# Kernel optimization log

Hardware: AMD Instinct MI355X
Metric: run time of the kernel (lower is better)

## Reference

```python
import jax, jax.numpy as jnp
import numpy as np

B, G, D, N_HEADS, FFN, L = 16, 2048, 256, 8, 1024, 4
HEAD_DIM = D // N_HEADS
EPS_LN = 1e-5
MASK_TOKEN = -10.0
REE_BASE = 100.0


def setup_inputs() -> dict:
    key = jax.random.key(0)
    ks = jax.random.split(key, 20)
    s = 0.02
    inp = {
        'x': jax.random.normal(ks[0], (B, G), jnp.float32),
        'gene_emb': jax.random.normal(ks[1], (G, D), jnp.float32) * s,
        'inv_freq': (1.0 / REE_BASE ** (jnp.arange(0, D, 2, dtype=jnp.float32) / D)),
        'Wq': jax.random.normal(ks[2], (L, D, D), jnp.float32) * s,
        'bq': jnp.zeros((L, D), jnp.float32),
        'Wk': jax.random.normal(ks[3], (L, D, D), jnp.float32) * s,
        'bk': jnp.zeros((L, D), jnp.float32),
        'Wv': jax.random.normal(ks[4], (L, D, D), jnp.float32) * s,
        'bv': jnp.zeros((L, D), jnp.float32),
        'ln1_g': jnp.ones((L, D), jnp.float32),
        'ln1_b': jnp.zeros((L, D), jnp.float32),
        'ln2_g': jnp.ones((L, D), jnp.float32),
        'ln2_b': jnp.zeros((L, D), jnp.float32),
        'WU': jax.random.normal(ks[5], (L, D, FFN), jnp.float32) * s,
        'bU': jnp.zeros((L, FFN), jnp.float32),
        'WV': jax.random.normal(ks[6], (L, FFN, D), jnp.float32) * s,
        'bV': jnp.zeros((L, D), jnp.float32),
        'Wout': jax.random.normal(ks[7], (D, 1), jnp.float32) * s,
        'bout': jnp.zeros((1,), jnp.float32),
    }
    return inp


def layernorm(x, g, b):
    m = x.mean(-1, keepdims=True)
    v = ((x - m) ** 2).mean(-1, keepdims=True)
    return (x - m) / jnp.sqrt(v + EPS_LN) * g + b


def causal_linear_attention(q, k, v):
    # q, k already feature-mapped ('sqr'); shapes [B, S, H, dh]
    b, s, h, dh = q.shape
    qs, ks_, vs = (jnp.moveaxis(t, 1, 0) for t in (q, k, v))  # [S,B,H,dh]
    num0 = jnp.zeros((b, h, dh, dh), q.dtype)
    den0 = jnp.zeros((b, h, dh), q.dtype)

    def step(carry, qkv):
        num_s, den_s = carry
        qt, kt, vt = qkv
        num_s = num_s + jnp.einsum('bhf,bhd->bhfd', kt, vt)
        den_s = den_s + kt
        num = jnp.einsum('bhf,bhfd->bhd', qt, num_s)
        den = jnp.einsum('bhf,bhf->bh', qt, den_s)
        return (num_s, den_s), num / (den[..., None] + 1e-16)

    _, out = jax.lax.scan(step, (num0, den0), (qs, ks_, vs))  # [S,B,H,dh]
    return jnp.moveaxis(out, 0, 1).reshape(b, s, h * dh)


def reference(x, gene_emb, inv_freq, Wq, bq, Wk, bk, Wv, bv,
              ln1_g, ln1_b, ln2_g, ln2_b, WU, bU, WV, bV, Wout, bout):
    b, g = x.shape
    # Rotary Expression Embedding
    freqs = x[..., None] * inv_freq  # [B,G,D/2]
    emb = jnp.concatenate([jnp.sin(freqs), jnp.cos(freqs)], axis=-1)  # [B,G,D]
    emb = jnp.where((x == MASK_TOKEN)[..., None], 0.0, emb)
    h = gene_emb[None] + emb  # [B,G,D]

    for l in range(Wq.shape[0]):
        hn = layernorm(h, ln1_g[l], ln1_b[l])  # pre-LN (on_gptln=True)
        q = (hn @ Wq[l] + bq[l]).reshape(b, g, N_HEADS, HEAD_DIM) ** 2
        k = (hn @ Wk[l] + bk[l]).reshape(b, g, N_HEADS, HEAD_DIM) ** 2
        v = (hn @ Wv[l] + bv[l]).reshape(b, g, N_HEADS, HEAD_DIM)
        h = h + causal_linear_attention(q, k, v)
        hn2 = layernorm(h, ln2_g[l], ln2_b[l])
        h = h + jax.nn.gelu(hn2 @ WU[l] + bU[l], approximate=False) @ WV[l] + bV[l]
    return (h @ Wout + bout).squeeze(-1)  # [B,G]
```

## Files before the change

### kernel.cpp

```cpp
#include <hip/hip_runtime.h>
#include <math.h>


#define GG 2048
#define DD 256
#define NROWS 32768
#define NC 32
#define CS 64

typedef __attribute__((ext_vector_type(8))) short bf16x8;
typedef __attribute__((ext_vector_type(4))) float f32x4;

__device__ __forceinline__ short f2bf(float f) {
  union { float f; unsigned u; } v; v.f = f;
  unsigned r = v.u + 0x7FFFu + ((v.u >> 16) & 1u);
  return (short)(r >> 16);
}
__device__ __forceinline__ float bf2f(short s) {
  union { unsigned u; float f; } v; v.u = ((unsigned)(unsigned short)s) << 16;
  return v.f;
}
__device__ __forceinline__ void gld16(const short* g, short* l) {
  __builtin_amdgcn_global_load_lds(
      (const __attribute__((address_space(1))) void*)g,
      (__attribute__((address_space(3))) void*)l, 16, 0, 0);
}
__device__ __forceinline__ float fast_gelu(float x) {
  float y = 1.595769122f * (x + 0.044715f * x * x * x);
  return x / (1.0f + __expf(-y));
}

__global__ __launch_bounds__(256) void embed_kernel(
    const float* __restrict__ x, const float* __restrict__ ge,
    const float* __restrict__ invf, float* __restrict__ h) {
  int bg = blockIdx.x * 4 + (threadIdx.x >> 6);
  int g = bg & (GG - 1);
  int lane = threadIdx.x & 63;
  float xv = x[bg];
  int d = lane * 4;
  float4 e;
  if (lane < 32) {
    float4 f = *(const float4*)&invf[d];
    e.x = sinf(xv * f.x); e.y = sinf(xv * f.y);
    e.z = sinf(xv * f.z); e.w = sinf(xv * f.w);
  } else {
    float4 f = *(const float4*)&invf[d - 128];
    e.x = cosf(xv * f.x); e.y = cosf(xv * f.y);
    e.z = cosf(xv * f.z); e.w = cosf(xv * f.w);
  }
  if (xv == -10.0f) { e.x = 0.f; e.y = 0.f; e.z = 0.f; e.w = 0.f; }
  float4 gv = *(const float4*)&ge[(size_t)g * DD + d];
  float4 o; o.x = gv.x + e.x; o.y = gv.y + e.y; o.z = gv.z + e.z; o.w = gv.w + e.w;
  *(float4*)&h[(size_t)bg * DD + d] = o;
}

__global__ __launch_bounds__(256) void ln_tiled(
    const float* __restrict__ h, const float* __restrict__ gamma,
    const float* __restrict__ beta, short* __restrict__ outT) {
  __shared__ float mean_s[32], rstd_s[32];
  __shared__ float gls[256], bls[256];
  int r0 = blockIdx.x * 32;
  int tid = threadIdx.x;
  gls[tid] = gamma[tid]; bls[tid] = beta[tid];
  {
    int row = tid >> 3, seg = tid & 7;
    const float4* hp = (const float4*)(h + (size_t)(r0 + row) * DD + seg * 32);
    float s = 0.f, s2 = 0.f;
#pragma unroll
    for (int i = 0; i < 8; ++i) {
      float4 v = hp[i];
      s += v.x + v.y + v.z + v.w;
      s2 += v.x * v.x + v.y * v.y + v.z * v.z + v.w * v.w;
    }
    s += __shfl_xor(s, 1); s += __shfl_xor(s, 2); s += __shfl_xor(s, 4);
    s2 += __shfl_xor(s2, 1); s2 += __shfl_xor(s2, 2); s2 += __shfl_xor(s2, 4);
    if (seg == 0) {
      float mn = s * (1.0f / 256.0f);
      mean_s[row] = mn;
      rstd_s[row] = rsqrtf(s2 * (1.0f / 256.0f) - mn * mn + 1e-5f);
    }
  }
  __syncthreads();
  int row = tid & 31, kc8 = (tid >> 5) & 3, half = tid >> 7;
  float mn = mean_s[row], rs = rstd_s[row];
  size_t hrow = (size_t)(r0 + row) * DD;
  int trow = (r0 & 127) + row;
  short* tb = outT + (size_t)(r0 >> 7) * 8 * 4096 + (kc8 * 128 + trow) * 8;
#pragma unroll
  for (int j = 0; j < 4; ++j) {
    int kb = half * 4 + j;
    int k0 = kb * 32 + kc8 * 8;
    float4 x0 = *(const float4*)&h[hrow + k0];
    float4 x1 = *(const float4*)&h[hrow + k0 + 4];
    float4 g0 = *(const float4*)&gls[k0], g1 = *(const float4*)&gls[k0 + 4];
    float4 b0 = *(const float4*)&bls[k0], b1 = *(const float4*)&bls[k0 + 4];
    bf16x8 aw;
    aw[0] = f2bf((x0.x - mn) * rs * g0.x + b0.x);
    aw[1] = f2bf((x0.y - mn) * rs * g0.y + b0.y);
    aw[2] = f2bf((x0.z - mn) * rs * g0.z + b0.z);
    aw[3] = f2bf((x0.w - mn) * rs * g0.w + b0.w);
    aw[4] = f2bf((x1.x - mn) * rs * g1.x + b1.x);
    aw[5] = f2bf((x1.y - mn) * rs * g1.y + b1.y);
    aw[6] = f2bf((x1.z - mn) * rs * g1.z + b1.z);
    aw[7] = f2bf((x1.w - mn) * rs * g1.w + b1.w);
    *(bf16x8*)&tb[(size_t)kb * 4096] = aw;
  }
}

__global__ __launch_bounds__(256) void prep_weights(
    const float* __restrict__ Wq, const float* __restrict__ Wk,
    const float* __restrict__ Wv, const float* __restrict__ WU,
    const float* __restrict__ WV,
    short* __restrict__ TQ, short* __restrict__ TK, short* __restrict__ TV,
    short* __restrict__ TU, short* __restrict__ TVd) {
  int zz = blockIdx.z, l = blockIdx.y;
  const float* src; short* dst; int Kd, Nd;
  if (zz == 0) { src = Wq; dst = TQ; Kd = 256; Nd = 256; }
  else if (zz == 1) { src = Wk; dst = TK; Kd = 256; Nd = 256; }
  else if (zz == 2) { src = Wv; dst = TV; Kd = 256; Nd = 256; }
  else if (zz == 3) { src = WU; dst = TU; Kd = 256; Nd = 1024; }
  else { src = WV; dst = TVd; Kd = 1024; Nd = 256; }
  int tot = Kd * Nd;
  int e = blockIdx.x * 256 + threadIdx.x;
  if (e >= tot) return;
  int t = e >> 12;
  int cslot = (e >> 3) & 511;
  int elem = e & 7;
  int kc8 = cslot >> 7, rn = cslot & 127;
  int nKb = Kd >> 5;
  int nt = t / nKb, kb = t - nt * nKb;
  int n = nt * 128 + rn, k = kb * 32 + kc8 * 8 + elem;
  dst[(size_t)l * tot + e] = f2bf(src[(size_t)l * tot + (size_t)k * Nd + n]);
}

template <int K, int EPI>
__global__ __launch_bounds__(256) void gemm_t(
    const short* __restrict__ A, const short* __restrict__ B0,
    const short* __restrict__ B1, const short* __restrict__ B2,
    const float* __restrict__ bias0, const float* __restrict__ bias1,
    const float* __restrict__ bias2,
    short* __restrict__ o0, short* __restrict__ o1, short* __restrict__ o2,
    float* __restrict__ outf, int N) {
  __shared__ __align__(16) short As[2][4096];
  __shared__ __align__(16) short Bs[2][4096];
  constexpr int nIter = K / 32;
  int z = blockIdx.z;
  const short* Bt = (z == 0) ? B0 : (z == 1) ? B1 : B2;
  const float* bias = (z == 0) ? bias0 : (z == 1) ? bias1 : bias2;
  short* outz = (z == 0) ? o0 : (z == 1) ? o1 : o2;
  int m0 = blockIdx.x * 128, n0 = blockIdx.y * 128;
  int tid = threadIdx.x;
  int lane = tid & 63, w = tid >> 6;
  int q = lane >> 4, r = lane & 15;
  int wm = (w >> 1) * 64, wn = (w & 1) * 64;
  const short* At = A + (size_t)blockIdx.x * nIter * 4096;
  const short* Btl = Bt + (size_t)blockIdx.y * nIter * 4096;
  f32x4 vzero = {0.f, 0.f, 0.f, 0.f};
  f32x4 acc[4][4];
#pragma unroll
  for (int i = 0; i < 4; ++i)
#pragma unroll
    for (int j = 0; j < 4; ++j) acc[i][j] = vzero;

  int c0 = tid * 8, c1 = (tid + 256) * 8;
#pragma unroll
  for (int g = 0; g < 2; ++g) {
    gld16(At + g * 4096 + c0, &As[g][c0]);
    gld16(At + g * 4096 + c1, &As[g][c1]);
    gld16(Btl + g * 4096 + c0, &Bs[g][c0]);
    gld16(Btl + g * 4096 + c1, &Bs[g][c1]);
  }

  int abase = (q * 128 + wm + r) * 8;
  int bbase = (q * 128 + wn + r) * 8;

#pragma unroll
  for (int gi = 0; gi < nIter - 1; ++gi) {
    __builtin_amdgcn_s_waitcnt(0x0f74);
    __builtin_amdgcn_s_barrier();
    const int cur = gi & 1;
    bf16x8 af[4], bfr[4];
#pragma unroll
    for (int mt = 0; mt < 4; ++mt)
      af[mt] = *(const bf16x8*)&As[cur][abase + mt * 16 * 8];
#pragma unroll
    for (int nt = 0; nt < 4; ++nt)
      bfr[nt] = *(const bf16x8*)&Bs[cur][bbase + nt * 16 * 8];
#pragma unroll
    for (int mt = 0; mt < 4; ++mt)
#pragma unroll
      for (int nt = 0; nt < 4; ++nt)
        acc[mt][nt] = __builtin_amdgcn_mfma_f32_16x16x32_bf16(bfr[nt], af[mt], acc[mt][nt], 0, 0, 0);
    __builtin_amdgcn_s_waitcnt(0xc07f);
    __builtin_amdgcn_s_barrier();
    if (gi + 2 < nIter) {
      size_t kn = (size_t)(gi + 2) * 4096;
      gld16(At + kn + c0, &As[cur][c0]);
      gld16(At + kn + c1, &As[cur][c1]);
      gld16(Btl + kn + c0, &Bs[cur][c0]);
      gld16(Btl + kn + c1, &Bs[cur][c1]);
    }
  }
  {
    __builtin_amdgcn_s_waitcnt(0x0f70);
    __builtin_amdgcn_s_barrier();
    const int cur = (nIter - 1) & 1;
    bf16x8 af[4], bfr[4];
#pragma unroll
    for (int mt = 0; mt < 4; ++mt)
      af[mt] = *(const bf16x8*)&As[cur][abase + mt * 16 * 8];
#pragma unroll
    for (int nt = 0; nt < 4; ++nt)
      bfr[nt] = *(const bf16x8*)&Bs[cur][bbase + nt * 16 * 8];
#pragma unroll
    for (int mt = 0; mt < 4; ++mt)
#pragma unroll
      for (int nt = 0; nt < 4; ++nt)
        acc[mt][nt] = __builtin_amdgcn_mfma_f32_16x16x32_bf16(bfr[nt], af[mt], acc[mt][nt], 0, 0, 0);
  }

  float4 bias4[4];
#pragma unroll
  for (int nt = 0; nt < 4; ++nt) bias4[nt] = *(const float4*)&bias[n0 + wn + nt * 16 + q * 4];
#pragma unroll
  for (int mt = 0; mt < 4; ++mt) {
    int ml = wm + mt * 16 + r;
    int m = m0 + ml;
    size_t rowoff = (size_t)m * N + n0 + wn + q * 4;
#pragma unroll
    for (int nt = 0; nt < 4; ++nt) {
      f32x4 v = acc[mt][nt];
      v[0] += bias4[nt].x; v[1] += bias4[nt].y; v[2] += bias4[nt].z; v[3] += bias4[nt].w;
      if (EPI == 0) {
        if (z < 2) { v[0] *= v[0]; v[1] *= v[1]; v[2] *= v[2]; v[3] *= v[3]; }
        short4 o; o.x = f2bf(v[0]); o.y = f2bf(v[1]); o.z = f2bf(v[2]); o.w = f2bf(v[3]);
        *(short4*)&outz[rowoff + nt * 16] = o;
      } else if (EPI == 1) {
#pragma unroll
        for (int e = 0; e < 4; ++e) v[e] = fast_gelu(v[e]);
        short4 o; o.x = f2bf(v[0]); o.y = f2bf(v[1]); o.z = f2bf(v[2]); o.w = f2bf(v[3]);
        int n = n0 + wn + nt * 16 + q * 4;
        size_t ti = ((size_t)blockIdx.x * (N >> 5) + (n >> 5)) * 4096 +
                    (size_t)(((n >> 3) & 3) << 10) + (ml << 3) + (n & 7);
        *(short4*)&outz[ti] = o;
      } else {
        float4 cur4 = *(float4*)&outf[rowoff + nt * 16];
        cur4.x += v[0]; cur4.y += v[1]; cur4.z += v[2]; cur4.w += v[3];
        *(float4*)&outf[rowoff + nt * 16] = cur4;
      }
    }
  }
}

__global__ __launch_bounds__(256) void attn_chunk_kv(
    const short* __restrict__ Kb, const short* __restrict__ Vb,
    float* __restrict__ St, float* __restrict__ Zc) {
  __shared__ short Kt[4][32 * 72];
  __shared__ short Vt[4][32 * 72];
  int wid = threadIdx.x >> 6;
  int blk = blockIdx.x * 4 + wid;
  int c = blk & (NC - 1), bh = blk >> 5;
  int b = bh >> 3, hh = bh & 7;
  int lane = threadIdx.x & 63, q = lane >> 4, r = lane & 15;
  size_t rowbase = ((size_t)(b * GG + c * CS + lane)) * DD + hh * 32;
#pragma unroll
  for (int j = 0; j < 4; ++j) {
    bf16x8 kv = *(const bf16x8*)&Kb[rowbase + j * 8];
    bf16x8 vv = *(const bf16x8*)&Vb[rowbase + j * 8];
#pragma unroll
    for (int e = 0; e < 8; ++e) {
      Kt[wid][(j * 8 + e) * 72 + lane] = kv[e];
      Vt[wid][(j * 8 + e) * 72 + lane] = vv[e];
    }
  }
  __syncthreads();
  f32x4 vzero = {0.f, 0.f, 0.f, 0.f};
  f32x4 acc[2][2];
#pragma unroll
  for (int i = 0; i < 2; ++i)
#pragma unroll
    for (int j = 0; j < 2; ++j) acc[i][j] = vzero;
#pragma unroll
  for (int ks = 0; ks < 2; ++ks) {
    bf16x8 afr[2], bfr[2];
#pragma unroll
    for (int mt = 0; mt < 2; ++mt) afr[mt] = *(const bf16x8*)&Kt[wid][(mt * 16 + r) * 72 + ks * 32 + q * 8];
#pragma unroll
    for (int nt = 0; nt < 2; ++nt) bfr[nt] = *(const bf16x8*)&Vt[wid][(nt * 16 + r) * 72 + ks * 32 + q * 8];
#pragma unroll
    for (int mt = 0; mt < 2; ++mt)
#pragma unroll
      for (int nt = 0; nt < 2; ++nt)
        acc[mt][nt] = __builtin_amdgcn_mfma_f32_16x16x32_bf16(afr[mt], bfr[nt], acc[mt][nt], 0, 0, 0);
  }
  float* stp = St + ((size_t)bh * NC + c) * 1024;
#pragma unroll
  for (int mt = 0; mt < 2; ++mt)
#pragma unroll
    for (int nt = 0; nt < 2; ++nt)
      *(f32x4*)&stp[(nt * 16 + r) * 32 + mt * 16 + q * 4] = acc[mt][nt];
  if (lane < 32) {
    float s = 0.f;
#pragma unroll
    for (int j = 0; j < 8; ++j) {
      bf16x8 kr = *(const bf16x8*)&Kt[wid][lane * 72 + j * 8];
#pragma unroll
      for (int e = 0; e < 8; ++e) s += bf2f(kr[e]);
    }
    Zc[((size_t)bh * NC + c) * 32 + lane] = s;
  }
}

__global__ __launch_bounds__(1024) void attn_prefix(float* __restrict__ St, float* __restrict__ Zc) {
  int bh = blockIdx.x, i = threadIdx.x;
  float run = 0.f;
  float* p = St + (size_t)bh * NC * 1024 + i;
#pragma unroll
  for (int c = 0; c < NC; ++c) { float t = p[(size_t)c * 1024]; p[(size_t)c * 1024] = run; run += t; }
  if (i < 32) {
    float rz = 0.f;
    float* pz = Zc + (size_t)bh * NC * 32 + i;
#pragma unroll
    for (int c = 0; c < NC; ++c) { float t = pz[c * 32]; pz[c * 32] = rz; rz += t; }
  }
}

__global__ __launch_bounds__(256) void attn_intra(
    const short* __restrict__ Qb, const short* __restrict__ Kb,
    const short* __restrict__ Vb, const float* __restrict__ St,
    const float* __restrict__ Zc, float* __restrict__ h) {
  __shared__ short P[4][64 * 72];
  __shared__ short Vt[4][32 * 72];
  __shared__ float den[4][64];
  int wid = threadIdx.x >> 6;
  int blk = blockIdx.x * 4 + wid;
  int c = blk & (NC - 1), bh = blk >> 5;
  int b = bh >> 3, hh = bh & 7;
  int lane = threadIdx.x & 63, q = lane >> 4, r = lane & 15;
  size_t row0 = (size_t)b * GG + c * CS;

  const float* zp = Zc + ((size_t)bh * NC + c) * 32;
  float qz = 0.f;
  {
    size_t qoff = (row0 + lane) * DD + hh * 32;
#pragma unroll
    for (int j = 0; j < 4; ++j) {
      bf16x8 qv = *(const bf16x8*)&Qb[qoff + j * 8];
#pragma unroll
      for (int e = 0; e < 8; ++e) qz += bf2f(qv[e]) * zp[j * 8 + e];
    }
  }
  den[wid][lane] = qz;

  {
    size_t voff = (row0 + lane) * DD + hh * 32;
#pragma unroll
    for (int j = 0; j < 4; ++j) {
      bf16x8 vv = *(const bf16x8*)&Vb[voff + j * 8];
#pragma unroll
      for (int e = 0; e < 8; ++e) Vt[wid][(j * 8 + e) * 72 + lane] = vv[e];
    }
  }

  bf16x8 ak[4], bqf[4];
#pragma unroll
  for (int t4 = 0; t4 < 4; ++t4) {
    ak[t4]  = *(const bf16x8*)&Kb[(row0 + t4 * 16 + r) * DD + hh * 32 + q * 8];
    bqf[t4] = *(const bf16x8*)&Qb[(row0 + t4 * 16 + r) * DD + hh * 32 + q * 8];
  }
  f32x4 vzero = {0.f, 0.f, 0.f, 0.f};
  f32x4 pacc[4][4];
#pragma unroll
  for (int mt = 0; mt < 4; ++mt)
#pragma unroll
    for (int nt = 0; nt < 4; ++nt)
      pacc[mt][nt] = __builtin_amdgcn_mfma_f32_16x16x32_bf16(ak[mt], bqf[nt], vzero, 0, 0, 0);

  float rs[4] = {0.f, 0.f, 0.f, 0.f};
#pragma unroll
  for (int nt = 0; nt < 4; ++nt) {
    int t = nt * 16 + r;
#pragma unroll
    for (int mt = 0; mt < 4; ++mt) {
      short4 pk;
#pragma unroll
      for (int rr = 0; rr < 4; ++rr) {
        int s = mt * 16 + q * 4 + rr;
        float pv = (s <= t) ? pacc[mt][nt][rr] : 0.f;
        rs[nt] += pv;
        ((short*)&pk)[rr] = f2bf(pv);
      }
      *(short4*)&P[wid][t * 72 + mt * 16 + q * 4] = pk;
    }
  }
#pragma unroll
  for (int nt = 0; nt < 4; ++nt) {
    rs[nt] += __shfl_xor(rs[nt], 16);
    rs[nt] += __shfl_xor(rs[nt], 32);
  }
  __syncthreads();
  if (lane < 16) {
#pragma unroll
    for (int nt = 0; nt < 4; ++nt) den[wid][nt * 16 + lane] += rs[nt];
  }
  __syncthreads();

  f32x4 oacc[4][2];
#pragma unroll
  for (int mt = 0; mt < 4; ++mt)
#pragma unroll
    for (int nt2 = 0; nt2 < 2; ++nt2) oacc[mt][nt2] = vzero;
  const float* stp = St + ((size_t)bh * NC + c) * 1024;
#pragma unroll
  for (int nt2 = 0; nt2 < 2; ++nt2) {
    float4 s0 = *(const float4*)&stp[(nt2 * 16 + r) * 32 + q * 8];
    float4 s1 = *(const float4*)&stp[(nt2 * 16 + r) * 32 + q * 8 + 4];
    bf16x8 bs;
    bs[0] = f2bf(s0.x); bs[1] = f2bf(s0.y); bs[2] = f2bf(s0.z); bs[3] = f2bf(s0.w);
    bs[4] = f2bf(s1.x); bs[5] = f2bf(s1.y); bs[6] = f2bf(s1.z); bs[7] = f2bf(s1.w);
#pragma unroll
    for (int mt = 0; mt < 4; ++mt)
      oacc[mt][nt2] = __builtin_amdgcn_mfma_f32_16x16x32_bf16(bqf[mt], bs, oacc[mt][nt2], 0, 0, 0);
  }
#pragma unroll
  for (int ks = 0; ks < 2; ++ks) {
    bf16x8 ap[4];
#pragma unroll
    for (int mt = 0; mt < 4; ++mt)
      ap[mt] = *(const bf16x8*)&P[wid][(mt * 16 + r) * 72 + ks * 32 + q * 8];
#pragma unroll
    for (int nt2 = 0; nt2 < 2; ++nt2) {
      bf16x8 bv_ = *(const bf16x8*)&Vt[wid][(nt2 * 16 + r) * 72 + ks * 32 + q * 8];
#pragma unroll
      for (int mt = 0; mt < 4; ++mt)
        oacc[mt][nt2] = __builtin_amdgcn_mfma_f32_16x16x32_bf16(ap[mt], bv_, oacc[mt][nt2], 0, 0, 0);
    }
  }

#pragma unroll
  for (int mt = 0; mt < 4; ++mt) {
#pragma unroll
    for (int rr = 0; rr < 4; ++rr) {
      int t = mt * 16 + q * 4 + rr;
      float inv = 1.0f / (den[wid][t] + 1e-16f);
#pragma unroll
      for (int nt2 = 0; nt2 < 2; ++nt2) {
        int d = nt2 * 16 + r;
        size_t off = (row0 + t) * DD + hh * 32 + d;
        h[off] += oacc[mt][nt2][rr] * inv;
      }
    }
  }
}

__global__ __launch_bounds__(256) void out_proj(
    const float* __restrict__ h, const float* __restrict__ Wout,
    const float* __restrict__ bout, float* __restrict__ out) {
  int row = blockIdx.x * 4 + (threadIdx.x >> 6);
  int lane = threadIdx.x & 63;
  float4 a = *(const float4*)&h[(size_t)row * DD + lane * 4];
  float4 w = *(const float4*)&Wout[lane * 4];
  float s = a.x * w.x + a.y * w.y + a.z * w.z + a.w * w.w;
#pragma unroll
  for (int o = 1; o < 64; o <<= 1) s += __shfl_xor(s, o);
  if (lane == 0) out[row] = s + bout[0];
}

extern "C" void kernel_launch(void* const* d_in, const int* in_sizes, int n_in,
                              void* d_out, int out_size, void* d_ws, size_t ws_size,
                              hipStream_t stream) {
  const float* x    = (const float*)d_in[0];
  const float* ge   = (const float*)d_in[1];
  const float* invf = (const float*)d_in[2];
  const float* Wq   = (const float*)d_in[3];
  const float* bq   = (const float*)d_in[4];
  const float* Wk   = (const float*)d_in[5];
  const float* bk   = (const float*)d_in[6];
  const float* Wv   = (const float*)d_in[7];
  const float* bv   = (const float*)d_in[8];
  const float* ln1g = (const float*)d_in[9];
  const float* ln1b = (const float*)d_in[10];
  const float* ln2g = (const float*)d_in[11];
  const float* ln2b = (const float*)d_in[12];
  const float* WU   = (const float*)d_in[13];
  const float* bU   = (const float*)d_in[14];
  const float* WV   = (const float*)d_in[15];
  const float* bV   = (const float*)d_in[16];
  const float* Wout = (const float*)d_in[17];
  const float* bout = (const float*)d_in[18];
  float* out = (float*)d_out;

  char* ws = (char*)d_ws;
  float* h   = (float*)(ws + 0);
  short* hn  = (short*)(ws + 33554432);
  char*  R   = ws + 50331648;
  short* qb  = (short*)(R + 0);
  short* kb  = (short*)(R + 16777216);
  short* vb  = (short*)(R + 33554432);
  float* St  = (float*)(R + 50331648);
  float* Zc  = (float*)(R + 67108864);
  short* mid = (short*)(R + 0);
  char*  WT  = R + 67633152;
  short* TQ  = (short*)(WT + 0);
  short* TK  = (short*)(WT + 524288);
  short* TVq = (short*)(WT + 1048576);
  short* TU  = (short*)(WT + 1572864);
  short* TVd = (short*)(WT + 3670016);

  prep_weights<<<dim3(1024, 4, 5), 256, 0, stream>>>(Wq, Wk, Wv, WU, WV, TQ, TK, TVq, TU, TVd);
  embed_kernel<<<NROWS / 4, 256, 0, stream>>>(x, ge, invf, h);

  for (int l = 0; l < 4; ++l) {
    ln_tiled<<<NROWS / 32, 256, 0, stream>>>(h, ln1g + l * 256, ln1b + l * 256, hn);
    gemm_t<256, 0><<<dim3(256, 2, 3), 256, 0, stream>>>(
        hn, TQ + l * 65536, TK + l * 65536, TVq + l * 65536,
        bq + l * 256, bk + l * 256, bv + l * 256,
        qb, kb, vb, nullptr, 256);
    attn_chunk_kv<<<1024, 256, 0, stream>>>(kb, vb, St, Zc);
    attn_prefix<<<128, 1024, 0, stream>>>(St, Zc);
    attn_intra<<<1024, 256, 0, stream>>>(qb, kb, vb, St, Zc, h);
    ln_tiled<<<NROWS / 32, 256, 0, stream>>>(h, ln2g + l * 256, ln2b + l * 256, hn);
    gemm_t<256, 1><<<dim3(256, 8, 1), 256, 0, stream>>>(
        hn, TU + l * 262144, nullptr, nullptr,
        bU + l * 1024, nullptr, nullptr,
        mid, nullptr, nullptr, nullptr, 1024);
    gemm_t<1024, 2><<<dim3(256, 2, 1), 256, 0, stream>>>(
        mid, TVd + l * 262144, nullptr, nullptr,
        bV + l * 256, nullptr, nullptr,
        nullptr, nullptr, nullptr, h, 256);
  }
  out_proj<<<NROWS / 4, 256, 0, stream>>>(h, Wout, bout, out);
}
```

Baseline: 790.3 us.

## Triple-buffer GEMM K-loop, stage epilogues through LDS, head-major QKV layout

The GEMM main loop moves from double to triple buffering of A/B tiles in a single shared array, with the wait count chosen by how many tiles are still outstanding. The QKV epilogue now stages results in LDS and writes head-major [head][row][32] bf16 so the attention kernels read contiguous 64-byte rows. The residual-add epilogue also stages through LDS in two halves so the fp32 read-modify-write of h is done with full-row coalesced float4 accesses. The aim is to hide more load latency and coalesce global traffic, at the cost of more LDS (lower occupancy) and extra barriers in the epilogues.

Result: faster. 762.5 us (-3.5%).

```diff
diff --git a/kernel.cpp b/kernel.cpp
--- a/kernel.cpp
+++ b/kernel.cpp
@@ -141,8 +141,7 @@
     const float* __restrict__ bias2,
     short* __restrict__ o0, short* __restrict__ o1, short* __restrict__ o2,
     float* __restrict__ outf, int N) {
-  __shared__ __align__(16) short As[2][4096];
-  __shared__ __align__(16) short Bs[2][4096];
+  __shared__ __align__(16) short L[24576];
   constexpr int nIter = K / 32;
   int z = blockIdx.z;
   const short* Bt = (z == 0) ? B0 : (z == 1) ? B1 : B2;
@@ -164,28 +163,33 @@
 
   int c0 = tid * 8, c1 = (tid + 256) * 8;
 #pragma unroll
-  for (int g = 0; g < 2; ++g) {
-    gld16(At + g * 4096 + c0, &As[g][c0]);
-    gld16(At + g * 4096 + c1, &As[g][c1]);
-    gld16(Btl + g * 4096 + c0, &Bs[g][c0]);
-    gld16(Btl + g * 4096 + c1, &Bs[g][c1]);
+  for (int g = 0; g < 3; ++g) {
+    gld16(At + g * 4096 + c0, &L[g * 4096 + c0]);
+    gld16(At + g * 4096 + c1, &L[g * 4096 + c1]);
+    gld16(Btl + g * 4096 + c0, &L[12288 + g * 4096 + c0]);
+    gld16(Btl + g * 4096 + c1, &L[12288 + g * 4096 + c1]);
   }
 
   int abase = (q * 128 + wm + r) * 8;
   int bbase = (q * 128 + wn + r) * 8;
 
 #pragma unroll
-  for (int gi = 0; gi < nIter - 1; ++gi) {
-    __builtin_amdgcn_s_waitcnt(0x0f74);
+  for (int gi = 0; gi < nIter; ++gi) {
+    const int rem = nIter - 1 - gi;
+    if (rem >= 2)      __builtin_amdgcn_s_waitcnt(0x0f78);
+    else if (rem == 1) __builtin_amdgcn_s_waitcnt(0x0f74);
+    else               __builtin_amdgcn_s_waitcnt(0x0f70);
     __builtin_amdgcn_s_barrier();
-    const int cur = gi & 1;
+    const int cur = gi % 3;
+    const short* Asc = &L[cur * 4096];
+    const short* Bsc = &L[12288 + cur * 4096];
     bf16x8 af[4], bfr[4];
 #pragma unroll
     for (int mt = 0; mt < 4; ++mt)
-      af[mt] = *(const bf16x8*)&As[cur][abase + mt * 16 * 8];
+      af[mt] = *(const bf16x8*)&Asc[abase + mt * 16 * 8];
 #pragma unroll
     for (int nt = 0; nt < 4; ++nt)
-      bfr[nt] = *(const bf16x8*)&Bs[cur][bbase + nt * 16 * 8];
+      bfr[nt] = *(const bf16x8*)&Bsc[bbase + nt * 16 * 8];
 #pragma unroll
     for (int mt = 0; mt < 4; ++mt)
 #pragma unroll
@@ -193,49 +197,51 @@
         acc[mt][nt] = __builtin_amdgcn_mfma_f32_16x16x32_bf16(bfr[nt], af[mt], acc[mt][nt], 0, 0, 0);
     __builtin_amdgcn_s_waitcnt(0xc07f);
     __builtin_amdgcn_s_barrier();
-    if (gi + 2 < nIter) {
-      size_t kn = (size_t)(gi + 2) * 4096;
-      gld16(At + kn + c0, &As[cur][c0]);
-      gld16(At + kn + c1, &As[cur][c1]);
-      gld16(Btl + kn + c0, &Bs[cur][c0]);
-      gld16(Btl + kn + c1, &Bs[cur][c1]);
-    }
-  }
-  {
-    __builtin_amdgcn_s_waitcnt(0x0f70);
-    __builtin_amdgcn_s_barrier();
-    const int cur = (nIter - 1) & 1;
-    bf16x8 af[4], bfr[4];
-#pragma unroll
-    for (int mt = 0; mt < 4; ++mt)
-      af[mt] = *(const bf16x8*)&As[cur][abase + mt * 16 * 8];
-#pragma unroll
-    for (int nt = 0; nt < 4; ++nt)
-      bfr[nt] = *(const bf16x8*)&Bs[cur][bbase + nt * 16 * 8];
-#pragma unroll
-    for (int mt = 0; mt < 4; ++mt)
-#pragma unroll
-      for (int nt = 0; nt < 4; ++nt)
-        acc[mt][nt] = __builtin_amdgcn_mfma_f32_16x16x32_bf16(bfr[nt], af[mt], acc[mt][nt], 0, 0, 0);
+    if (gi + 3 < nIter) {
+      size_t kn = (size_t)(gi + 3) * 4096;
+      gld16(At + kn + c0, &L[cur * 4096 + c0]);
+      gld16(At + kn + c1, &L[cur * 4096 + c1]);
+      gld16(Btl + kn + c0, &L[12288 + cur * 4096 + c0]);
+      gld16(Btl + kn + c1, &L[12288 + cur * 4096 + c1]);
+    }
   }
 
   float4 bias4[4];
 #pragma unroll
   for (int nt = 0; nt < 4; ++nt) bias4[nt] = *(const float4*)&bias[n0 + wn + nt * 16 + q * 4];
-#pragma unroll
-  for (int mt = 0; mt < 4; ++mt) {
-    int ml = wm + mt * 16 + r;
-    int m = m0 + ml;
-    size_t rowoff = (size_t)m * N + n0 + wn + q * 4;
-#pragma unroll
-    for (int nt = 0; nt < 4; ++nt) {
-      f32x4 v = acc[mt][nt];
-      v[0] += bias4[nt].x; v[1] += bias4[nt].y; v[2] += bias4[nt].z; v[3] += bias4[nt].w;
-      if (EPI == 0) {
+
+  if (EPI == 0) {
+    short* T = L;
+#pragma unroll
+    for (int mt = 0; mt < 4; ++mt) {
+      int ml = wm + mt * 16 + r;
+#pragma unroll
+      for (int nt = 0; nt < 4; ++nt) {
+        f32x4 v = acc[mt][nt];
+        v[0] += bias4[nt].x; v[1] += bias4[nt].y; v[2] += bias4[nt].z; v[3] += bias4[nt].w;
         if (z < 2) { v[0] *= v[0]; v[1] *= v[1]; v[2] *= v[2]; v[3] *= v[3]; }
-        short4 o; o.x = f2bf(v[0]); o.y = f2bf(v[1]); o.z = f2bf(v[2]); o.w = f2bf(v[3]);
-        *(short4*)&outz[rowoff + nt * 16] = o;
-      } else if (EPI == 1) {
+        short4 pk; pk.x = f2bf(v[0]); pk.y = f2bf(v[1]); pk.z = f2bf(v[2]); pk.w = f2bf(v[3]);
+        *(short4*)&T[ml * 132 + wn + nt * 16 + q * 4] = pk;
+      }
+    }
+    __syncthreads();
+#pragma unroll
+    for (int t2 = 0; t2 < 2; ++t2) {
+      int task = tid + t2 * 256;
+      int row = task & 127, hl = task >> 7;
+      size_t obase = ((size_t)((n0 >> 5) + hl) * NROWS + m0 + row) * 32;
+#pragma unroll
+      for (int j = 0; j < 4; ++j)
+        *(bf16x8*)&outz[obase + j * 8] = *(const bf16x8*)&T[row * 132 + hl * 32 + j * 8];
+    }
+  } else if (EPI == 1) {
+#pragma unroll
+    for (int mt = 0; mt < 4; ++mt) {
+      int ml = wm + mt * 16 + r;
+#pragma unroll
+      for (int nt = 0; nt < 4; ++nt) {
+        f32x4 v = acc[mt][nt];
+        v[0] += bias4[nt].x; v[1] += bias4[nt].y; v[2] += bias4[nt].z; v[3] += bias4[nt].w;
 #pragma unroll
         for (int e = 0; e < 4; ++e) v[e] = fast_gelu(v[e]);
         short4 o; o.x = f2bf(v[0]); o.y = f2bf(v[1]); o.z = f2bf(v[2]); o.w = f2bf(v[3]);
@@ -243,10 +249,34 @@
         size_t ti = ((size_t)blockIdx.x * (N >> 5) + (n >> 5)) * 4096 +
                     (size_t)(((n >> 3) & 3) << 10) + (ml << 3) + (n & 7);
         *(short4*)&outz[ti] = o;
-      } else {
-        float4 cur4 = *(float4*)&outf[rowoff + nt * 16];
-        cur4.x += v[0]; cur4.y += v[1]; cur4.z += v[2]; cur4.w += v[3];
-        *(float4*)&outf[rowoff + nt * 16] = cur4;
+      }
+    }
+  } else {
+    float* TF = (float*)L;
+#pragma unroll
+    for (int half = 0; half < 2; ++half) {
+      __syncthreads();
+      if ((w & 1) == half) {
+#pragma unroll
+        for (int mt = 0; mt < 4; ++mt) {
+          int ml = wm + mt * 16 + r;
+#pragma unroll
+          for (int nt = 0; nt < 4; ++nt) {
+            f32x4 v = acc[mt][nt];
+            v[0] += bias4[nt].x; v[1] += bias4[nt].y; v[2] += bias4[nt].z; v[3] += bias4[nt].w;
+            *(f32x4*)&TF[ml * 68 + nt * 16 + q * 4] = v;
+          }
+        }
+      }
+      __syncthreads();
+      int row = tid >> 1, col = (tid & 1) * 32;
+      size_t hoff = (size_t)(m0 + row) * N + n0 + half * 64 + col;
+#pragma unroll
+      for (int j = 0; j < 8; ++j) {
+        float4 add = *(const float4*)&TF[row * 68 + col + j * 4];
+        float4 cur4 = *(float4*)&outf[hoff + j * 4];
+        cur4.x += add.x; cur4.y += add.y; cur4.z += add.z; cur4.w += add.w;
+        *(float4*)&outf[hoff + j * 4] = cur4;
       }
     }
   }
@@ -262,7 +292,7 @@
   int c = blk & (NC - 1), bh = blk >> 5;
   int b = bh >> 3, hh = bh & 7;
   int lane = threadIdx.x & 63, q = lane >> 4, r = lane & 15;
-  size_t rowbase = ((size_t)(b * GG + c * CS + lane)) * DD + hh * 32;
+  size_t rowbase = ((size_t)hh * NROWS + b * GG + c * CS + lane) * 32;
 #pragma unroll
   for (int j = 0; j < 4; ++j) {
     bf16x8 kv = *(const bf16x8*)&Kb[rowbase + j * 8];
@@ -337,12 +367,13 @@
   int c = blk & (NC - 1), bh = blk >> 5;
   int b = bh >> 3, hh = bh & 7;
   int lane = threadIdx.x & 63, q = lane >> 4, r = lane & 15;
-  size_t row0 = (size_t)b * GG + c * CS;
+  size_t hrow0 = (size_t)b * GG + c * CS;
+  size_t qrow0 = (size_t)hh * NROWS + b * GG + c * CS;
 
   const float* zp = Zc + ((size_t)bh * NC + c) * 32;
   float qz = 0.f;
   {
-    size_t qoff = (row0 + lane) * DD + hh * 32;
+    size_t qoff = (qrow0 + lane) * 32;
 #pragma unroll
     for (int j = 0; j < 4; ++j) {
       bf16x8 qv = *(const bf16x8*)&Qb[qoff + j * 8];
@@ -353,7 +384,7 @@
   den[wid][lane] = qz;
 
   {
-    size_t voff = (row0 + lane) * DD + hh * 32;
+    size_t voff = (qrow0 + lane) * 32;
 #pragma unroll
     for (int j = 0; j < 4; ++j) {
       bf16x8 vv = *(const bf16x8*)&Vb[voff + j * 8];
@@ -365,8 +396,8 @@
   bf16x8 ak[4], bqf[4];
 #pragma unroll
   for (int t4 = 0; t4 < 4; ++t4) {
-    ak[t4]  = *(const bf16x8*)&Kb[(row0 + t4 * 16 + r) * DD + hh * 32 + q * 8];
-    bqf[t4] = *(const bf16x8*)&Qb[(row0 + t4 * 16 + r) * DD + hh * 32 + q * 8];
+    ak[t4]  = *(const bf16x8*)&Kb[(qrow0 + t4 * 16 + r) * 32 + q * 8];
+    bqf[t4] = *(const bf16x8*)&Qb[(qrow0 + t4 * 16 + r) * 32 + q * 8];
   }
   f32x4 vzero = {0.f, 0.f, 0.f, 0.f};
   f32x4 pacc[4][4];
@@ -446,7 +477,7 @@
 #pragma unroll
       for (int nt2 = 0; nt2 < 2; ++nt2) {
         int d = nt2 * 16 + r;
-        size_t off = (row0 + t) * DD + hh * 32 + d;
+        size_t off = (hrow0 + t) * DD + hh * 32 + d;
         h[off] += oacc[mt][nt2][rr] * inv;
       }
     }
```
